# Optimization experiments

Hardware: AMD Instinct MI355X
Metric: run time of the kernel (lower is better)

## Reference

```python
import jax, jax.numpy as jnp
import numpy as np

B, S, D, C, H, E, K, L = 32, 512, 768, 3072, 1024, 8, 2, 2


def _layernorm(x, g, b, eps=1e-5):
    mu = jnp.mean(x, axis=-1, keepdims=True)
    var = jnp.var(x, axis=-1, keepdims=True)
    return (x - mu) * jax.lax.rsqrt(var + eps) * g + b


def setup_inputs() -> dict:
    key = jax.random.key(0)
    ks = jax.random.split(key, 12)
    s = 0.02
    return {
        "hidden_states": jax.random.normal(ks[0], (B, S, C), jnp.float32),
        "proj_w": jax.random.normal(ks[1], (C, D), jnp.float32) * s,
        "proj_b": jnp.zeros((D,), jnp.float32),
        "ln1_g": jnp.ones((D,), jnp.float32),
        "ln1_b": jnp.zeros((D,), jnp.float32),
        "gate_w": jax.random.normal(ks[2], (D, E), jnp.float32) * s,
        "gate_b": jnp.zeros((E,), jnp.float32),
        "w1": jax.random.normal(ks[3], (E, D, H), jnp.float32) * s,
        "b1": jnp.zeros((E, H), jnp.float32),
        "w2": jax.random.normal(ks[4], (E, H, D), jnp.float32) * s,
        "b2": jnp.zeros((E, D), jnp.float32),
        "ln2_g": jnp.ones((D,), jnp.float32),
        "ln2_b": jnp.zeros((D,), jnp.float32),
        "cls_w": jax.random.normal(ks[5], (D, L), jnp.float32) * s,
        "cls_b": jnp.zeros((L,), jnp.float32),
    }


def reference(hidden_states, proj_w, proj_b, ln1_g, ln1_b, gate_w, gate_b,
              w1, b1, w2, b2, ln2_g, ln2_b, cls_w, cls_b):
    # layer_projection: Linear -> LayerNorm -> GELU (dropout = identity in eval)
    x = jnp.einsum('bsc,cd->bsd', hidden_states, proj_w) + proj_b
    x = _layernorm(x, ln1_g, ln1_b)
    seq_out = jax.nn.gelu(x, approximate=False)  # [B,S,D]

    # Router: gate -> softmax -> top-k -> renormalize
    probs = jax.nn.softmax(seq_out @ gate_w + gate_b, axis=-1)  # [B,S,E]
    top_w, top_i = jax.lax.top_k(probs, K)                      # [B,S,K]
    top_w = top_w / jnp.sum(top_w, axis=-1, keepdims=True)

    # combine[t,e] = sum_k top_w[t,k] * (top_i[t,k]==e)
    combine = jnp.sum(jax.nn.one_hot(top_i, E, dtype=top_w.dtype)
                      * top_w[..., None], axis=-2)              # [B,S,E]

    xt = seq_out.reshape(-1, D)                                 # [T,D]
    ct = combine.reshape(-1, E)                                 # [T,E]
    h = jax.nn.gelu(jnp.einsum('td,edh->eth', xt, w1) + b1[:, None, :],
                    approximate=False)                          # [E,T,H]
    eo = jnp.einsum('eth,ehd->etd', h, w2) + b2[:, None, :]     # [E,T,D]
    moe = jnp.einsum('etd,te->td', eo, ct).reshape(B, S, D)

    moe = _layernorm(moe + seq_out, ln2_g, ln2_b)
    logits = moe @ cls_w + cls_b                                # [B,S,2]
    return logits
```

## Files before the change

### kernel.cpp

```cpp
#include <hip/hip_runtime.h>
#include <hip/hip_bf16.h>

#define T_TOK 16384
#define CDIM 3072
#define DDIM 768
#define HDIM 1024
#define NEXP 8
#define NSLOT 33792
#define MAXTILE 264
#define AMB_CAP 2048
#define AMB2_CAP 256
#define KSPLIT 4
#define NSEG 8

typedef __attribute__((ext_vector_type(8))) short bfrag;
typedef __attribute__((ext_vector_type(4))) float f32x4;
typedef __attribute__((ext_vector_type(4))) float fvec4;

__device__ __forceinline__ unsigned short bf16_rn(float f) {
  union { float f; unsigned u; } v; v.f = f;
  unsigned r = v.u + 0x7fffu + ((v.u >> 16) & 1u);
  return (unsigned short)(r >> 16);
}
__device__ __forceinline__ float bf16_f32(unsigned short h) {
  union { unsigned u; float f; } v; v.u = ((unsigned)h) << 16;
  return v.f;
}
__device__ __forceinline__ float gelu_exact(float x) {
  return 0.5f * x * (1.0f + erff(x * 0.70710678118654752440f));
}
__device__ __forceinline__ void glds16(const void* g, void* l) {
  __builtin_amdgcn_global_load_lds((const __attribute__((address_space(1))) void*)g,
                                   (__attribute__((address_space(3))) void*)l, 16, 0, 0);
}

__global__ void k_init(int* token_list, int* counts, int* cursors, unsigned short* zero_row,
                       int* amb_count, int* amb2_count) {
  int i = blockIdx.x * 256 + threadIdx.x;
  for (int j = i; j < NSLOT; j += 64 * 256) token_list[j] = -1;
  if (i < NEXP) counts[i] = 0;
  if (i < 128) cursors[i] = 0;
  if (i == 0) { *amb_count = 0; *amb2_count = 0; }
  if (i < 1024) zero_row[i] = 0;
}

__global__ void k_cast_tiled(const float* __restrict__ src,
                             unsigned short* __restrict__ dst) {
  __shared__ unsigned short h[128][136];
  int rb = blockIdx.x;
  int cc = blockIdx.y;
  int tid = threadIdx.x;
  const float* in = src + ((size_t)rb * 128) * CDIM + cc * 128;
#pragma unroll
  for (int it = 0; it < 16; ++it) {
    int idx = it * 256 + tid;
    int r = idx >> 5, nv = idx & 31;
    fvec4 v = *(const fvec4*)(in + (size_t)r * CDIM + nv * 4);
    unsigned long long p = (unsigned long long)bf16_rn(v[0]) |
                           ((unsigned long long)bf16_rn(v[1]) << 16) |
                           ((unsigned long long)bf16_rn(v[2]) << 32) |
                           ((unsigned long long)bf16_rn(v[3]) << 48);
    *(unsigned long long*)&h[r][nv * 4] = p;
  }
  __syncthreads();
  unsigned short* ob = dst + ((size_t)rb * 96 + cc * 4) * 4096;
#pragma unroll
  for (int kt = 0; kt < 4; ++kt) {
#pragma unroll
    for (int it = 0; it < 2; ++it) {
      int gg = it * 256 + tid;
      int kg = gg >> 7, r = gg & 127;
      bfrag o = *(const bfrag*)&h[r][kt * 32 + kg * 8];
      *(bfrag*)(ob + ((size_t)kt * 512 + gg) * 8) = o;
    }
  }
}

__global__ void k_transpose_split(const float* __restrict__ src,
                                  unsigned short* __restrict__ dhi,
                                  unsigned short* __restrict__ dlo) {
  __shared__ unsigned short h[128][72], l[128][72];
  int nb2 = blockIdx.x;
  int cb = blockIdx.y;
  int col_blk = nb2 >> 1, nhalf = nb2 & 1;
  int n0 = col_blk * 128 + nhalf * 64;
  int tid = threadIdx.x;
  const float* in = src + (size_t)(cb * 128) * DDIM + n0;
#pragma unroll
  for (int it = 0; it < 8; ++it) {
    int idx = it * 256 + tid;
    int cl = idx >> 4, nv = idx & 15;
    fvec4 v = *(const fvec4*)(in + (size_t)cl * DDIM + nv * 4);
    unsigned long long ph = 0, pl = 0;
#pragma unroll
    for (int e = 0; e < 4; ++e) {
      unsigned short hh = bf16_rn(v[e]);
      unsigned short ll = bf16_rn(v[e] - bf16_f32(hh));
      ph |= (unsigned long long)hh << (16 * e);
      pl |= (unsigned long long)ll << (16 * e);
    }
    *(unsigned long long*)&h[cl][nv * 4] = ph;
    *(unsigned long long*)&l[cl][nv * 4] = pl;
  }
  __syncthreads();
  size_t obase = ((size_t)col_blk * 96 + cb * 4) * 4096;
#pragma unroll
  for (int kt = 0; kt < 4; ++kt) {
    int kg = tid >> 6, rl = tid & 63;
    bfrag oh, ol;
#pragma unroll
    for (int e = 0; e < 8; ++e) {
      int c = kt * 32 + kg * 8 + e;
      oh[e] = (short)h[c][rl];
      ol[e] = (short)l[c][rl];
    }
    size_t gi = obase + ((size_t)kt * 512 + kg * 128 + nhalf * 64 + rl) * 8;
    *(bfrag*)(dhi + gi) = oh;
    *(bfrag*)(dlo + gi) = ol;
  }
}

__global__ void k_transpose_tiled(const float* __restrict__ src0,
                                  unsigned short* __restrict__ dst0, int K, int N) {
  __shared__ unsigned short h[128][72];
  int nb2 = blockIdx.x;
  int cb = blockIdx.y;
  int z = blockIdx.z;
  int col_blk = nb2 >> 1, nhalf = nb2 & 1;
  int n0 = col_blk * 128 + nhalf * 64;
  int tid = threadIdx.x;
  const float* in = src0 + (size_t)z * K * N + (size_t)(cb * 128) * N + n0;
#pragma unroll
  for (int it = 0; it < 8; ++it) {
    int idx = it * 256 + tid;
    int cl = idx >> 4, nv = idx & 15;
    fvec4 v = *(const fvec4*)(in + (size_t)cl * N + nv * 4);
    unsigned long long ph = 0;
#pragma unroll
    for (int e = 0; e < 4; ++e)
      ph |= (unsigned long long)bf16_rn(v[e]) << (16 * e);
    *(unsigned long long*)&h[cl][nv * 4] = ph;
  }
  __syncthreads();
  size_t obase = (size_t)z * K * N + ((size_t)col_blk * (K / 32) + cb * 4) * 4096;
#pragma unroll
  for (int kt = 0; kt < 4; ++kt) {
    int kg = tid >> 6, rl = tid & 63;
    bfrag oh;
#pragma unroll
    for (int e = 0; e < 8; ++e) oh[e] = (short)h[kt * 32 + kg * 8 + e][rl];
    *(bfrag*)(dst0 + obase + ((size_t)kt * 512 + kg * 128 + nhalf * 64 + rl) * 8) = oh;
  }
}

__launch_bounds__(256, 3)
__global__ void k_gemm1(const unsigned short* __restrict__ Atil,
                        const unsigned short* __restrict__ Btil,
                        float* __restrict__ Cout)
{
  __shared__ unsigned short sA[12288], sB[12288];
  int tid = threadIdx.x;
  int lane = tid & 63, wave = tid >> 6;
  int id = blockIdx.x;
  int swz = (id & 7) * 96 + (id >> 3);
  int brow = swz / 6, bcol = swz % 6;
  int row0 = brow * 128, col0 = bcol * 128;
  int wm = wave >> 1, wn = wave & 1;

  f32x4 acc[4][4];
#pragma unroll
  for (int i = 0; i < 4; ++i)
#pragma unroll
    for (int j = 0; j < 4; ++j) acc[i][j] = (f32x4){0.f, 0.f, 0.f, 0.f};

  int rsel = lane & 15, kq = lane >> 4;
  const unsigned short* At = Atil + (size_t)(brow * 96) * 4096;
  const unsigned short* Bt = Btil + (size_t)(bcol * 96) * 4096;

  auto STAGE = [&](int kt, int b) {
    const unsigned short* as = At + (size_t)kt * 4096;
    const unsigned short* bs = Bt + (size_t)kt * 4096;
    int lbase = b * 4096;
#pragma unroll
    for (int pass = 0; pass < 2; ++pass) {
      int g = pass * 256 + tid;
      int li = lbase + (pass * 256 + wave * 64) * 8;
      glds16(as + (size_t)g * 8, &sA[li]);
      glds16(bs + (size_t)g * 8, &sB[li]);
    }
  };

  STAGE(0, 0);
  STAGE(1, 1);
  int b0 = 0;
  for (int kt = 0; kt < 96; ++kt) {
    if (kt < 95) asm volatile("s_waitcnt vmcnt(4)" ::: "memory");
    else         asm volatile("s_waitcnt vmcnt(0)" ::: "memory");
    __builtin_amdgcn_s_barrier();
    if (kt + 2 < 96) {
      int bn = b0 + 2; if (bn >= 3) bn -= 3;
      STAGE(kt + 2, bn);
    }
    int lb = b0 * 4096;
    bfrag af[4], bf[4];
#pragma unroll
    for (int i = 0; i < 4; ++i) {
      af[i] = *(const bfrag*)&sA[lb + (kq * 128 + wm * 64 + i * 16 + rsel) * 8];
      bf[i] = *(const bfrag*)&sB[lb + (kq * 128 + wn * 64 + i * 16 + rsel) * 8];
    }
#pragma unroll
    for (int i = 0; i < 4; ++i)
#pragma unroll
      for (int j = 0; j < 4; ++j)
        acc[i][j] = __builtin_amdgcn_mfma_f32_16x16x32_bf16(af[i], bf[j], acc[i][j], 0, 0, 0);
    b0 = (b0 == 2) ? 0 : b0 + 1;
  }

  int cc = lane & 15, rr = (lane >> 4) * 4;
#pragma unroll
  for (int i = 0; i < 4; ++i)
#pragma unroll
    for (int j = 0; j < 4; ++j)
#pragma unroll
      for (int r = 0; r < 4; ++r) {
        int row = row0 + wm * 64 + i * 16 + rr + r;
        int col = col0 + wn * 64 + j * 16 + cc;
        Cout[(size_t)row * DDIM + col] = acc[i][j][r];
      }
}

__launch_bounds__(256)
__global__ void k_ln_router(const float* __restrict__ xw, const float* __restrict__ proj_b,
                            const float* __restrict__ g1, const float* __restrict__ b1v,
                            const float* __restrict__ gate_w, const float* __restrict__ gate_b,
                            unsigned short* __restrict__ seq_b16,
                            int* __restrict__ top_i, float* __restrict__ top_w,
                            int* __restrict__ amb_list, int* __restrict__ amb_count)
{
  int lane = threadIdx.x & 63;
  int t = blockIdx.x * 4 + (threadIdx.x >> 6);
  const float* xr = xw + (size_t)t * DDIM;
  float x0[12];
  float s = 0.f, s2 = 0.f;
#pragma unroll
  for (int j = 0; j < 12; ++j) {
    int d = lane + 64 * j;
    float v = xr[d] + proj_b[d];
    x0[j] = v; s += v; s2 += v * v;
  }
#pragma unroll
  for (int o = 32; o > 0; o >>= 1) { s += __shfl_xor(s, o, 64); s2 += __shfl_xor(s2, o, 64); }
  float mu = s * (1.f / DDIM);
  float rstd = rsqrtf(s2 * (1.f / DDIM) - mu * mu + 1e-5f);
  float acc8[8];
#pragma unroll
  for (int e = 0; e < 8; ++e) acc8[e] = 0.f;
#pragma unroll
  for (int j = 0; j < 12; ++j) {
    int d = lane + 64 * j;
    float y = (x0[j] - mu) * rstd * g1[d] + b1v[d];
    float ge = gelu_exact(y);
    seq_b16[(size_t)t * DDIM + d] = bf16_rn(ge);
    const float* gw = gate_w + (size_t)d * NEXP;
#pragma unroll
    for (int e = 0; e < 8; ++e) acc8[e] += ge * gw[e];
  }
#pragma unroll
  for (int e = 0; e < 8; ++e)
#pragma unroll
    for (int o = 32; o > 0; o >>= 1) acc8[e] += __shfl_xor(acc8[e], o, 64);
  if (lane == 0) {
    float lg[8];
#pragma unroll
    for (int e = 0; e < 8; ++e) lg[e] = acc8[e] + gate_b[e];
    int i0 = 0;
    for (int e = 1; e < 8; ++e) if (lg[e] > lg[i0]) i0 = e;
    int i1 = (i0 == 0) ? 1 : 0;
    for (int e = 0; e < 8; ++e) if (e != i0 && lg[e] > lg[i1]) i1 = e;
    float l2 = -1e30f;
    for (int e = 0; e < 8; ++e) if (e != i0 && e != i1 && lg[e] > l2) l2 = lg[e];
    if (lg[i1] - l2 < 8e-3f) {
      int p = atomicAdd(amb_count, 1);
      if (p < AMB_CAP) amb_list[p] = t;
    }
    float w0 = 1.f / (1.f + expf(lg[i1] - lg[i0]));
    top_i[t * 2] = i0; top_i[t * 2 + 1] = i1;
    top_w[t * 2] = w0; top_w[t * 2 + 1] = 1.f - w0;
  }
}

__launch_bounds__(256, 2)
__global__ void k_repair(const float* __restrict__ hidden,
                         const unsigned short* __restrict__ BTh,
                         const unsigned short* __restrict__ BTl,
                         const int* __restrict__ amb_list, const int* __restrict__ amb_count,
                         float* __restrict__ xw_fix4)
{
  int n = *amb_count; if (n > AMB_CAP) n = AMB_CAP;
  int by = blockIdx.y;
  if (by * 128 >= n) return;
  int bx = blockIdx.x;
  int z = blockIdx.z;
  int col0 = bx * 128;
  __shared__ unsigned short sAh[8192], sAl[8192], sBh[8192], sBl[8192];
  __shared__ int tk[128];
  int tid = threadIdx.x, lane = tid & 63, wave = tid >> 6;
  if (tid < 128) tk[tid] = (by * 128 + tid < n) ? amb_list[by * 128 + tid] : -1;
  __syncthreads();
  int wm = wave >> 1, wn = wave & 1;
  f32x4 acc[4][4];
#pragma unroll
  for (int i = 0; i < 4; ++i)
#pragma unroll
    for (int j = 0; j < 4; ++j) acc[i][j] = (f32x4){0.f, 0.f, 0.f, 0.f};
  int rsel = lane & 15, kq = lane >> 4;
  int ktbase = z * 24;
  const unsigned short* Bth = BTh + (size_t)(bx * 96) * 4096;
  const unsigned short* Btl = BTl + (size_t)(bx * 96) * 4096;

  auto STAGE = [&](int kt, int b) {
    int k0 = (ktbase + kt) * 32;
    int lb = b * 4096;
    size_t tb = (size_t)(ktbase + kt) * 4096;
#pragma unroll
    for (int pass = 0; pass < 2; ++pass) {
      int g = pass * 256 + tid;
      int kg = g >> 7, r = g & 127;
      int tok = tk[r];
      fvec4 a0 = (fvec4){0.f, 0.f, 0.f, 0.f}, a1 = a0;
      if (tok >= 0) {
        const float* ap = hidden + (size_t)tok * CDIM + k0 + kg * 8;
        a0 = *(const fvec4*)ap;
        a1 = *(const fvec4*)(ap + 4);
      }
      bfrag hv, lv;
#pragma unroll
      for (int u = 0; u < 8; ++u) {
        float v = (u < 4) ? a0[u] : a1[u - 4];
        unsigned short h = bf16_rn(v);
        hv[u] = (short)h;
        lv[u] = (short)bf16_rn(v - bf16_f32(h));
      }
      *(bfrag*)&sAh[lb + (size_t)g * 8] = hv;
      *(bfrag*)&sAl[lb + (size_t)g * 8] = lv;
      int li = lb + (pass * 256 + wave * 64) * 8;
      glds16(Bth + tb + (size_t)g * 8, &sBh[li]);
      glds16(Btl + tb + (size_t)g * 8, &sBl[li]);
    }
  };

  STAGE(0, 0);
  __syncthreads();
  for (int kt = 0; kt < 24; ++kt) {
    int b = kt & 1;
    if (kt + 1 < 24) STAGE(kt + 1, b ^ 1);
    int lb = b * 4096;
    bfrag ah[4], al[4], bh[4], bl[4];
#pragma unroll
    for (int i = 0; i < 4; ++i) {
      int ra = wm * 64 + i * 16 + rsel;
      ah[i] = *(const bfrag*)&sAh[lb + (kq * 128 + ra) * 8];
      al[i] = *(const bfrag*)&sAl[lb + (kq * 128 + ra) * 8];
      int cb = wn * 64 + i * 16 + rsel;
      bh[i] = *(const bfrag*)&sBh[lb + (kq * 128 + cb) * 8];
      bl[i] = *(const bfrag*)&sBl[lb + (kq * 128 + cb) * 8];
    }
#pragma unroll
    for (int i = 0; i < 4; ++i)
#pragma unroll
      for (int j = 0; j < 4; ++j) {
        acc[i][j] = __builtin_amdgcn_mfma_f32_16x16x32_bf16(ah[i], bh[j], acc[i][j], 0, 0, 0);
        acc[i][j] = __builtin_amdgcn_mfma_f32_16x16x32_bf16(ah[i], bl[j], acc[i][j], 0, 0, 0);
        acc[i][j] = __builtin_amdgcn_mfma_f32_16x16x32_bf16(al[i], bh[j], acc[i][j], 0, 0, 0);
      }
    __syncthreads();
  }
  float* dst = xw_fix4 + (size_t)z * AMB_CAP * DDIM;
  int cc = lane & 15, rr = (lane >> 4) * 4;
#pragma unroll
  for (int i = 0; i < 4; ++i)
#pragma unroll
    for (int j = 0; j < 4; ++j)
#pragma unroll
      for (int r = 0; r < 4; ++r) {
        int row = by * 128 + wm * 64 + i * 16 + rr + r;
        int col = col0 + wn * 64 + j * 16 + cc;
        dst[(size_t)row * DDIM + col] = acc[i][j][r];
      }
}

__launch_bounds__(256)
__global__ void k_fix2(const float* __restrict__ xw_fix4, const float* __restrict__ proj_b,
                       const float* __restrict__ g1, const float* __restrict__ b1v,
                       const float* __restrict__ gate_w, const float* __restrict__ gate_b,
                       const int* __restrict__ amb_list, const int* __restrict__ amb_count,
                       int* __restrict__ top_i, float* __restrict__ top_w,
                       int* __restrict__ amb2_list, int* __restrict__ amb2_count)
{
  int n = *amb_count; if (n > AMB_CAP) n = AMB_CAP;
  int lane = threadIdx.x & 63;
  int slot = blockIdx.x * 4 + (threadIdx.x >> 6);
  if (slot >= n) return;
  int t = amb_list[slot];
  const float* p0 = xw_fix4 + (size_t)slot * DDIM;
  const float* p1 = p0 + (size_t)AMB_CAP * DDIM;
  const float* p2 = p1 + (size_t)AMB_CAP * DDIM;
  const float* p3 = p2 + (size_t)AMB_CAP * DDIM;
  float x0[12];
  float s = 0.f, s2 = 0.f;
#pragma unroll
  for (int j = 0; j < 12; ++j) {
    int d = lane + 64 * j;
    float v = ((p0[d] + p1[d]) + (p2[d] + p3[d])) + proj_b[d];
    x0[j] = v; s += v; s2 += v * v;
  }
#pragma unroll
  for (int o = 32; o > 0; o >>= 1) { s += __shfl_xor(s, o, 64); s2 += __shfl_xor(s2, o, 64); }
  float mu = s * (1.f / DDIM);
  float rstd = rsqrtf(s2 * (1.f / DDIM) - mu * mu + 1e-5f);
  float acc8[8];
#pragma unroll
  for (int e = 0; e < 8; ++e) acc8[e] = 0.f;
#pragma unroll
  for (int j = 0; j < 12; ++j) {
    int d = lane + 64 * j;
    float y = (x0[j] - mu) * rstd * g1[d] + b1v[d];
    float ge = gelu_exact(y);
    const float* gw = gate_w + (size_t)d * NEXP;
#pragma unroll
    for (int e = 0; e < 8; ++e) acc8[e] += ge * gw[e];
  }
#pragma unroll
  for (int e = 0; e < 8; ++e)
#pragma unroll
    for (int o = 32; o > 0; o >>= 1) acc8[e] += __shfl_xor(acc8[e], o, 64);
  if (lane == 0) {
    float lg[8];
#pragma unroll
    for (int e = 0; e < 8; ++e) lg[e] = acc8[e] + gate_b[e];
    int i0 = 0;
    for (int e = 1; e < 8; ++e) if (lg[e] > lg[i0]) i0 = e;
    int i1 = (i0 == 0) ? 1 : 0;
    for (int e = 0; e < 8; ++e) if (e != i0 && lg[e] > lg[i1]) i1 = e;
    float l2 = -1e30f;
    for (int e = 0; e < 8; ++e) if (e != i0 && e != i1 && lg[e] > l2) l2 = lg[e];
    if (lg[i1] - l2 < 2e-4f) {
      int p = atomicAdd(amb2_count, 1);
      if (p < AMB2_CAP) amb2_list[p] = t;
    }
    float w0 = 1.f / (1.f + expf(lg[i1] - lg[i0]));
    top_i[t * 2] = i0; top_i[t * 2 + 1] = i1;
    top_w[t * 2] = w0; top_w[t * 2 + 1] = 1.f - w0;
  }
}

__launch_bounds__(256, 1)
__global__ void k_router_fix(const float* __restrict__ hidden, const float* __restrict__ proj_w,
                             const int* __restrict__ amb2_list, const int* __restrict__ amb2_count,
                             double* __restrict__ xpart)
{
  __shared__ float hrow[384];
  int tid = threadIdx.x;
  int seg = blockIdx.y;
  int cbase = seg * 384;
  int n = *amb2_count; if (n > AMB2_CAP) n = AMB2_CAP;
  for (int ii = blockIdx.x; ii < n; ii += gridDim.x) {
    int t = amb2_list[ii];
    __syncthreads();
    if (tid < 96)
      *(fvec4*)&hrow[tid * 4] = *(const fvec4*)(hidden + (size_t)t * CDIM + cbase + tid * 4);
    __syncthreads();
    double p0a = 0.0, p0b = 0.0, p1a = 0.0, p1b = 0.0, p2a = 0.0, p2b = 0.0;
    for (int c0 = 0; c0 < 384; c0 += 16) {
      float w0r[16], w1r[16], w2r[16];
      const float* wp = proj_w + (size_t)(cbase + c0) * DDIM + tid;
#pragma unroll
      for (int u = 0; u < 16; ++u) {
        w0r[u] = wp[u * DDIM];
        w1r[u] = wp[u * DDIM + 256];
        w2r[u] = wp[u * DDIM + 512];
      }
#pragma unroll
      for (int u = 0; u < 16; ++u) {
        double h = (double)hrow[c0 + u];
        if (u & 1) { p0b += h * (double)w0r[u]; p1b += h * (double)w1r[u]; p2b += h * (double)w2r[u]; }
        else       { p0a += h * (double)w0r[u]; p1a += h * (double)w1r[u]; p2a += h * (double)w2r[u]; }
      }
    }
    double* xp = xpart + ((size_t)seg * AMB2_CAP + ii) * DDIM;
    xp[tid] = p0a + p0b;
    xp[tid + 256] = p1a + p1b;
    xp[tid + 512] = p2a + p2b;
  }
}

__launch_bounds__(256)
__global__ void k_fix3(const double* __restrict__ xpart, const float* __restrict__ proj_b,
                       const float* __restrict__ g1, const float* __restrict__ b1v,
                       const float* __restrict__ gate_w, const float* __restrict__ gate_b,
                       const int* __restrict__ amb2_list, const int* __restrict__ amb2_count,
                       int* __restrict__ top_i, float* __restrict__ top_w)
{
  __shared__ double redA[4], redB[4], red8[4][8];
  int n = *amb2_count; if (n > AMB2_CAP) n = AMB2_CAP;
  int ii = blockIdx.x;
  if (ii >= n) return;
  int t = amb2_list[ii];
  int tid = threadIdx.x, lane = tid & 63, wave = tid >> 6;
  double x[3]; double s = 0.0, s2 = 0.0;
#pragma unroll
  for (int j = 0; j < 3; ++j) {
    int d = tid + 256 * j;
    double acc = (double)proj_b[d];
#pragma unroll
    for (int seg = 0; seg < NSEG; ++seg)
      acc += xpart[((size_t)seg * AMB2_CAP + ii) * DDIM + d];
    x[j] = acc; s += acc; s2 += acc * acc;
  }
#pragma unroll
  for (int o = 32; o > 0; o >>= 1) { s += __shfl_down(s, o, 64); s2 += __shfl_down(s2, o, 64); }
  if (lane == 0) { redA[wave] = s; redB[wave] = s2; }
  __syncthreads();
  double mu = (redA[0] + redA[1] + redA[2] + redA[3]) / DDIM;
  double ms = (redB[0] + redB[1] + redB[2] + redB[3]) / DDIM;
  double rstd = 1.0 / sqrt(ms - mu * mu + 1e-5);
  double a8[8];
#pragma unroll
  for (int e = 0; e < 8; ++e) a8[e] = 0.0;
#pragma unroll
  for (int j = 0; j < 3; ++j) {
    int d = tid + 256 * j;
    double y = (x[j] - mu) * rstd * (double)g1[d] + (double)b1v[d];
    double ge = 0.5 * y * (1.0 + erf(y * 0.7071067811865475244));
#pragma unroll
    for (int e = 0; e < 8; ++e) a8[e] += ge * (double)gate_w[(size_t)d * NEXP + e];
  }
#pragma unroll
  for (int e = 0; e < 8; ++e)
#pragma unroll
    for (int o = 32; o > 0; o >>= 1) a8[e] += __shfl_down(a8[e], o, 64);
  if (lane == 0) {
#pragma unroll
    for (int e = 0; e < 8; ++e) red8[wave][e] = a8[e];
  }
  __syncthreads();
  if (tid == 0) {
    double lg[8];
#pragma unroll
    for (int e = 0; e < 8; ++e)
      lg[e] = red8[0][e] + red8[1][e] + red8[2][e] + red8[3][e] + (double)gate_b[e];
    int i0 = 0;
    for (int e = 1; e < 8; ++e) if (lg[e] > lg[i0]) i0 = e;
    int i1 = (i0 == 0) ? 1 : 0;
    for (int e = 0; e < 8; ++e) if (e != i0 && e != i1 && lg[e] > lg[i1]) i1 = e;
    double w0 = 1.0 / (1.0 + exp(lg[i1] - lg[i0]));
    top_i[t * 2] = i0; top_i[t * 2 + 1] = i1;
    top_w[t * 2] = (float)w0; top_w[t * 2 + 1] = (float)(1.0 - w0);
  }
}

__global__ void k_count(const int* __restrict__ top_i, int* __restrict__ counts) {
  __shared__ int h[NEXP];
  int tid = threadIdx.x;
  if (tid < NEXP) h[tid] = 0;
  __syncthreads();
  for (int i = blockIdx.x * 256 + tid; i < 2 * T_TOK; i += 64 * 256)
    atomicAdd(&h[top_i[i]], 1);
  __syncthreads();
  if (tid < NEXP) atomicAdd(&counts[tid], h[tid]);
}

__global__ void k_offsets(const int* __restrict__ counts, int* __restrict__ seg_start,
                          int* __restrict__ padded_total, int* __restrict__ tile_expert) {
  if (threadIdx.x != 0 || blockIdx.x != 0) return;
  int st[NEXP], en[NEXP];
  int s = 0;
  for (int e = 0; e < NEXP; ++e) {
    st[e] = s; seg_start[e] = s;
    s += (counts[e] + 127) & ~127;
    en[e] = s;
  }
  *padded_total = s;
  int nt = s >> 7;
  for (int x = 0; x < nt; ++x) {
    int r = x << 7, e = 0;
    for (int q = 0; q < NEXP; ++q) if (r >= st[q] && r < en[q]) e = q;
    tile_expert[x] = e;
  }
}

__global__ void k_scatter(const int* __restrict__ top_i, const int* __restrict__ seg_start,
                          int* __restrict__ cursors, int* __restrict__ token_list,
                          int* __restrict__ slot_of) {
  __shared__ int lc[NEXP];
  __shared__ int lbase[NEXP];
  int tid = threadIdx.x;
  int t = blockIdx.x * 256 + tid;
  if (tid < NEXP) lc[tid] = 0;
  __syncthreads();
  int e0 = top_i[t * 2], e1 = top_i[t * 2 + 1];
  int o0 = atomicAdd(&lc[e0], 1);
  int o1 = atomicAdd(&lc[e1], 1);
  __syncthreads();
  if (tid < NEXP) lbase[tid] = atomicAdd(&cursors[tid << 4], lc[tid]);
  __syncthreads();
  int p0 = seg_start[e0] + lbase[e0] + o0;
  int p1 = seg_start[e1] + lbase[e1] + o1;
  token_list[p0] = t;
  token_list[p1] = t;
  slot_of[t * 2] = p0;
  slot_of[t * 2 + 1] = p1;
}

__global__ void k_gather(const unsigned short* __restrict__ seqb,
                         const int* __restrict__ token_list,
                         const int* __restrict__ padded_total,
                         unsigned short* __restrict__ seqgT) {
  int sb = blockIdx.x;
  if (sb * 128 >= *padded_total) return;
  int cc = blockIdx.y;
  __shared__ unsigned short h[128][136];
  __shared__ int tk[128];
  int tid = threadIdx.x;
  if (tid < 128) tk[tid] = token_list[sb * 128 + tid];
  __syncthreads();
#pragma unroll
  for (int it = 0; it < 8; ++it) {
    int idx = it * 256 + tid;
    int r = idx >> 4, nv = idx & 15;
    int tok = tk[r];
    bfrag v = (bfrag){0, 0, 0, 0, 0, 0, 0, 0};
    if (tok >= 0)
      v = *(const bfrag*)(seqb + (size_t)tok * DDIM + cc * 128 + nv * 8);
    *(bfrag*)&h[r][nv * 8] = v;
  }
  __syncthreads();
  unsigned short* ob = seqgT + ((size_t)sb * 24 + cc * 4) * 4096;
#pragma unroll
  for (int kt = 0; kt < 4; ++kt) {
#pragma unroll
    for (int it = 0; it < 2; ++it) {
      int gg = it * 256 + tid;
      int kg = gg >> 7, r = gg & 127;
      bfrag o = *(const bfrag*)&h[r][kt * 32 + kg * 8];
      *(bfrag*)(ob + ((size_t)kt * 512 + gg) * 8) = o;
    }
  }
}

__launch_bounds__(256, 4)
__global__ void k_gemm2(const unsigned short* __restrict__ seqgT,
                        const unsigned short* __restrict__ w1T,
                        const float* __restrict__ b1,
                        const int* __restrict__ tile_expert,
                        const int* __restrict__ padded_total,
                        unsigned short* __restrict__ hbufT)
{
  int by = blockIdx.x;
  if (by * 128 >= *padded_total) return;
  int bx = blockIdx.y;
  int e = tile_expert[by];
  __shared__ unsigned short sA[8192], sB[8192];
  int tid = threadIdx.x, lane = tid & 63, wave = tid >> 6;
  int col0 = bx * 128;
  int wm = wave >> 1, wn = wave & 1;
  f32x4 acc[4][4];
#pragma unroll
  for (int i = 0; i < 4; ++i)
#pragma unroll
    for (int j = 0; j < 4; ++j) acc[i][j] = (f32x4){0.f, 0.f, 0.f, 0.f};
  const unsigned short* At = seqgT + (size_t)by * 24 * 4096;
  const unsigned short* Bt = w1T + (size_t)e * HDIM * DDIM + (size_t)bx * 24 * 4096;
  int rsel = lane & 15, kq = lane >> 4;

  auto STAGE = [&](int kt, int b) {
    int lbase2 = b * 4096;
    size_t tb = (size_t)kt * 4096;
#pragma unroll
    for (int pass = 0; pass < 2; ++pass) {
      int g = pass * 256 + tid;
      int li = lbase2 + (pass * 256 + wave * 64) * 8;
      glds16(At + tb + (size_t)g * 8, &sA[li]);
      glds16(Bt + tb + (size_t)g * 8, &sB[li]);
    }
  };

  STAGE(0, 0);
  __syncthreads();
  for (int kt = 0; kt < 24; ++kt) {
    int b = kt & 1;
    if (kt + 1 < 24) STAGE(kt + 1, b ^ 1);
    int lb = b * 4096;
    bfrag af[4], bf[4];
#pragma unroll
    for (int i = 0; i < 4; ++i) {
      af[i] = *(const bfrag*)&sA[lb + (kq * 128 + wm * 64 + i * 16 + rsel) * 8];
      bf[i] = *(const bfrag*)&sB[lb + (kq * 128 + wn * 64 + i * 16 + rsel) * 8];
    }
#pragma unroll
    for (int i = 0; i < 4; ++i)
#pragma unroll
      for (int j = 0; j < 4; ++j)
        acc[i][j] = __builtin_amdgcn_mfma_f32_16x16x32_bf16(af[i], bf[j], acc[i][j], 0, 0, 0);
    __syncthreads();
  }
  int cc = lane & 15, rr = (lane >> 4) * 4;
#pragma unroll
  for (int i = 0; i < 4; ++i)
#pragma unroll
    for (int j = 0; j < 4; ++j)
#pragma unroll
      for (int r = 0; r < 4; ++r) {
        int lr = wm * 64 + i * 16 + rr + r;
        int col = col0 + wn * 64 + j * 16 + cc;
        float x = acc[i][j][r] + b1[(size_t)e * HDIM + col];
        size_t tile = (size_t)by * 32 + (col >> 5);
        int g = ((col >> 3) & 3) * 128 + lr;
        hbufT[tile * 4096 + g * 8 + (col & 7)] = bf16_rn(gelu_exact(x));
      }
}

__launch_bounds__(256, 4)
__global__ void k_gemm3(const unsigned short* __restrict__ hbufT,
                        const unsigned short* __restrict__ w2T,
                        const float* __restrict__ b2,
                        const int* __restrict__ tile_expert,
                        const int* __restrict__ padded_total,
                        float* __restrict__ eo)
{
  int by = blockIdx.x;
  if (by * 128 >= *padded_total) return;
  int bx = blockIdx.y;
  int e = tile_expert[by];
  __shared__ unsigned short sA[8192], sB[8192];
  int tid = threadIdx.x, lane = tid & 63, wave = tid >> 6;
  int col0 = bx * 128;
  int wm = wave >> 1, wn = wave & 1;
  f32x4 acc[4][4];
#pragma unroll
  for (int i = 0; i < 4; ++i)
#pragma unroll
    for (int j = 0; j < 4; ++j) acc[i][j] = (f32x4){0.f, 0.f, 0.f, 0.f};
  const unsigned short* At = hbufT + (size_t)by * 32 * 4096;
  const unsigned short* Bt = w2T + (size_t)e * DDIM * HDIM + (size_t)bx * 32 * 4096;
  int rsel = lane & 15, kq = lane >> 4;

  auto STAGE = [&](int kt, int b) {
    int lbase2 = b * 4096;
    size_t tb = (size_t)kt * 4096;
#pragma unroll
    for (int pass = 0; pass < 2; ++pass) {
      int g = pass * 256 + tid;
      int li = lbase2 + (pass * 256 + wave * 64) * 8;
      glds16(At + tb + (size_t)g * 8, &sA[li]);
      glds16(Bt + tb + (size_t)g * 8, &sB[li]);
    }
  };

  STAGE(0, 0);
  __syncthreads();
  for (int kt = 0; kt < 32; ++kt) {
    int b = kt & 1;
    if (kt + 1 < 32) STAGE(kt + 1, b ^ 1);
    int lb = b * 4096;
    bfrag af[4], bf[4];
#pragma unroll
    for (int i = 0; i < 4; ++i) {
      af[i] = *(const bfrag*)&sA[lb + (kq * 128 + wm * 64 + i * 16 + rsel) * 8];
      bf[i] = *(const bfrag*)&sB[lb + (kq * 128 + wn * 64 + i * 16 + rsel) * 8];
    }
#pragma unroll
    for (int i = 0; i < 4; ++i)
#pragma unroll
      for (int j = 0; j < 4; ++j)
        acc[i][j] = __builtin_amdgcn_mfma_f32_16x16x32_bf16(af[i], bf[j], acc[i][j], 0, 0, 0);
    __syncthreads();
  }
  int cc = lane & 15, rr = (lane >> 4) * 4;
#pragma unroll
  for (int i = 0; i < 4; ++i)
#pragma unroll
    for (int j = 0; j < 4; ++j)
#pragma unroll
      for (int r = 0; r < 4; ++r) {
        int row = by * 128 + wm * 64 + i * 16 + rr + r;
        int col = col0 + wn * 64 + j * 16 + cc;
        eo[(size_t)row * DDIM + col] = acc[i][j][r] + b2[(size_t)e * DDIM + col];
      }
}

__launch_bounds__(256)
__global__ void k_combine(const float* __restrict__ eo, const unsigned short* __restrict__ seqb,
                          const int* __restrict__ slot_of, const float* __restrict__ top_w,
                          const float* __restrict__ g2, const float* __restrict__ b2v,
                          const float* __restrict__ cls_w, const float* __restrict__ cls_b,
                          float* __restrict__ out)
{
  int lane = threadIdx.x & 63;
  int t = blockIdx.x * 4 + (threadIdx.x >> 6);
  int s0 = slot_of[t * 2], s1 = slot_of[t * 2 + 1];
  float w0 = top_w[t * 2], w1 = top_w[t * 2 + 1];
  const float* p0 = eo + (size_t)s0 * DDIM;
  const float* p1 = eo + (size_t)s1 * DDIM;
  const unsigned short* sq = seqb + (size_t)t * DDIM;
  float m[12];
  float s = 0.f, s2 = 0.f;
#pragma unroll
  for (int j = 0; j < 12; ++j) {
    int d = lane + 64 * j;
    float v = w0 * p0[d] + w1 * p1[d] + bf16_f32(sq[d]);
    m[j] = v; s += v; s2 += v * v;
  }
#pragma unroll
  for (int o = 32; o > 0; o >>= 1) { s += __shfl_xor(s, o, 64); s2 += __shfl_xor(s2, o, 64); }
  float mu = s * (1.f / DDIM);
  float rstd = rsqrtf(s2 * (1.f / DDIM) - mu * mu + 1e-5f);
  float l0 = 0.f, l1 = 0.f;
#pragma unroll
  for (int j = 0; j < 12; ++j) {
    int d = lane + 64 * j;
    float y = (m[j] - mu) * rstd * g2[d] + b2v[d];
    l0 += y * cls_w[d * 2];
    l1 += y * cls_w[d * 2 + 1];
  }
#pragma unroll
  for (int o = 32; o > 0; o >>= 1) { l0 += __shfl_xor(l0, o, 64); l1 += __shfl_xor(l1, o, 64); }
  if (lane == 0) {
    out[(size_t)t * 2] = l0 + cls_b[0];
    out[(size_t)t * 2 + 1] = l1 + cls_b[1];
  }
}

extern "C" void kernel_launch(void* const* d_in, const int* in_sizes, int n_in,
                              void* d_out, int out_size, void* d_ws, size_t ws_size,
                              hipStream_t stream) {
  const float* hidden = (const float*)d_in[0];
  const float* proj_w = (const float*)d_in[1];
  const float* proj_b = (const float*)d_in[2];
  const float* ln1_g  = (const float*)d_in[3];
  const float* ln1_b  = (const float*)d_in[4];
  const float* gate_w = (const float*)d_in[5];
  const float* gate_b = (const float*)d_in[6];
  const float* w1     = (const float*)d_in[7];
  const float* b1     = (const float*)d_in[8];
  const float* w2     = (const float*)d_in[9];
  const float* b2     = (const float*)d_in[10];
  const float* ln2_g  = (const float*)d_in[11];
  const float* ln2_b  = (const float*)d_in[12];
  const float* cls_w  = (const float*)d_in[13];
  const float* cls_b  = (const float*)d_in[14];
  float* out = (float*)d_out;

  char* base = (char*)d_ws;
  size_t off = 0;
  auto alloc = [&](size_t b) -> void* {
    void* p = base + off;
    off += (b + 255) & ~(size_t)255;
    return p;
  };
  unsigned short* pwT_hi = (unsigned short*)alloc((size_t)DDIM * CDIM * 2);
  unsigned short* pwT_lo = (unsigned short*)alloc((size_t)DDIM * CDIM * 2);
  unsigned short* w1T    = (unsigned short*)alloc((size_t)NEXP * HDIM * DDIM * 2);
  unsigned short* w2T    = (unsigned short*)alloc((size_t)NEXP * DDIM * HDIM * 2);
  float* xw              = (float*)alloc((size_t)T_TOK * DDIM * 4);
  float* xw_fix4         = (float*)alloc((size_t)KSPLIT * AMB_CAP * DDIM * 4);
  double* xpart          = (double*)alloc((size_t)NSEG * AMB2_CAP * DDIM * 8);
  unsigned short* seqb   = (unsigned short*)alloc((size_t)T_TOK * DDIM * 2);
  unsigned short* seqgT  = (unsigned short*)alloc((size_t)MAXTILE * 24 * 4096 * 2);
  int* top_i             = (int*)alloc((size_t)T_TOK * 2 * 4);
  float* top_w           = (float*)alloc((size_t)T_TOK * 2 * 4);
  int* slot_of           = (int*)alloc((size_t)T_TOK * 2 * 4);
  int* amb_list          = (int*)alloc((size_t)AMB_CAP * 4);
  int* amb2_list         = (int*)alloc((size_t)AMB2_CAP * 4);
  int* token_list        = (int*)alloc((size_t)NSLOT * 4);
  int* counts            = (int*)alloc(256);
  int* cursors           = (int*)alloc(512);
  int* seg_start         = (int*)alloc(256);
  int* padded_total      = (int*)alloc(256);
  int* tile_expert       = (int*)alloc((size_t)MAXTILE * 4);
  unsigned short* zero_row = (unsigned short*)alloc(2048);
  int* amb_count         = (int*)alloc(256);
  int* amb2_count        = (int*)alloc(256);
  size_t poolBytes = 2 * (size_t)T_TOK * CDIM * 2;
  char* pool = (char*)alloc(poolBytes);
  unsigned short* Ahi = (unsigned short*)pool;
  size_t poff = 0;
  auto palloc = [&](size_t b) -> void* {
    void* p = pool + poff;
    poff += (b + 255) & ~(size_t)255;
    return p;
  };
  unsigned short* hbufT  = (unsigned short*)palloc((size_t)MAXTILE * 32 * 4096 * 2);
  float* eo              = (float*)palloc((size_t)NSLOT * DDIM * 4);
  (void)ws_size; (void)in_sizes; (void)n_in; (void)out_size;

  k_init<<<64, 256, 0, stream>>>(token_list, counts, cursors, zero_row, amb_count, amb2_count);
  k_cast_tiled<<<dim3(128, 24), 256, 0, stream>>>(hidden, Ahi);
  k_transpose_split<<<dim3(12, 24), 256, 0, stream>>>(proj_w, pwT_hi, pwT_lo);
  k_transpose_tiled<<<dim3(16, 6, 8), 256, 0, stream>>>(w1, w1T, DDIM, HDIM);
  k_transpose_tiled<<<dim3(12, 8, 8), 256, 0, stream>>>(w2, w2T, HDIM, DDIM);
  k_gemm1<<<768, 256, 0, stream>>>(Ahi, pwT_hi, xw);
  k_ln_router<<<T_TOK / 4, 256, 0, stream>>>(xw, proj_b, ln1_g, ln1_b, gate_w, gate_b,
                                             seqb, top_i, top_w, amb_list, amb_count);
  k_repair<<<dim3(6, AMB_CAP / 128, KSPLIT), 256, 0, stream>>>(hidden, pwT_hi, pwT_lo,
                                                               amb_list, amb_count, xw_fix4);
  k_fix2<<<AMB_CAP / 4, 256, 0, stream>>>(xw_fix4, proj_b, ln1_g, ln1_b, gate_w, gate_b,
                                          amb_list, amb_count, top_i, top_w,
                                          amb2_list, amb2_count);
  k_router_fix<<<dim3(64, NSEG), 256, 0, stream>>>(hidden, proj_w, amb2_list, amb2_count, xpart);
  k_fix3<<<AMB2_CAP, 256, 0, stream>>>(xpart, proj_b, ln1_g, ln1_b, gate_w, gate_b,
                                       amb2_list, amb2_count, top_i, top_w);
  k_count<<<64, 256, 0, stream>>>(top_i, counts);
  k_offsets<<<1, 64, 0, stream>>>(counts, seg_start, padded_total, tile_expert);
  k_scatter<<<64, 256, 0, stream>>>(top_i, seg_start, cursors, token_list, slot_of);
  k_gather<<<dim3(MAXTILE, 6), 256, 0, stream>>>(seqb, token_list, padded_total, seqgT);
  k_gemm2<<<dim3(MAXTILE, 8), 256, 0, stream>>>(seqgT, w1T, b1, tile_expert,
                                                padded_total, hbufT);
  k_gemm3<<<dim3(MAXTILE, 6), 256, 0, stream>>>(hbufT, w2T, b2, tile_expert, padded_total, eo);
  k_combine<<<T_TOK / 4, 256, 0, stream>>>(eo, seqb, slot_of, top_w, ln2_g, ln2_b,
                                           cls_w, cls_b, out);
}
```

Baseline: 631.7 us.

## Widen expert GEMM tiles to 128x256 and store expert outputs in bf16

Both expert GEMMs now compute 128x256 output tiles per block, with each wave covering 64x128, so A-tile loads are reused across twice as many columns and the grid's column dimension is halved. Launch bounds drop to 2 blocks per CU to make room for the larger accumulator array and doubled B shared memory. Separately, the expert output buffer is stored as bf16 instead of fp32, halving the write traffic in gemm3 and the read traffic in the combine kernel. The cost is fewer resident waves, fewer blocks to fill the GPU, and some loss of precision in the expert outputs.

```diff
diff --git a/kernel.cpp b/kernel.cpp
--- a/kernel.cpp
+++ b/kernel.cpp
@@ -648,7 +648,7 @@
   }
 }
 
-__launch_bounds__(256, 4)
+__launch_bounds__(256, 2)
 __global__ void k_gemm2(const unsigned short* __restrict__ seqgT,
                         const unsigned short* __restrict__ w1T,
                         const float* __restrict__ b1,
@@ -660,28 +660,32 @@
   if (by * 128 >= *padded_total) return;
   int bx = blockIdx.y;
   int e = tile_expert[by];
-  __shared__ unsigned short sA[8192], sB[8192];
+  __shared__ unsigned short sA[8192], sB[16384];
   int tid = threadIdx.x, lane = tid & 63, wave = tid >> 6;
-  int col0 = bx * 128;
   int wm = wave >> 1, wn = wave & 1;
-  f32x4 acc[4][4];
+  f32x4 acc[4][8];
 #pragma unroll
   for (int i = 0; i < 4; ++i)
 #pragma unroll
-    for (int j = 0; j < 4; ++j) acc[i][j] = (f32x4){0.f, 0.f, 0.f, 0.f};
+    for (int j = 0; j < 8; ++j) acc[i][j] = (f32x4){0.f, 0.f, 0.f, 0.f};
   const unsigned short* At = seqgT + (size_t)by * 24 * 4096;
-  const unsigned short* Bt = w1T + (size_t)e * HDIM * DDIM + (size_t)bx * 24 * 4096;
+  const unsigned short* Bt0 = w1T + (size_t)e * HDIM * DDIM + (size_t)(2 * bx) * 24 * 4096;
+  const unsigned short* Bt1 = Bt0 + (size_t)24 * 4096;
   int rsel = lane & 15, kq = lane >> 4;
 
   auto STAGE = [&](int kt, int b) {
-    int lbase2 = b * 4096;
     size_t tb = (size_t)kt * 4096;
 #pragma unroll
-    for (int pass = 0; pass < 2; ++pass) {
-      int g = pass * 256 + tid;
-      int li = lbase2 + (pass * 256 + wave * 64) * 8;
-      glds16(At + tb + (size_t)g * 8, &sA[li]);
-      glds16(Bt + tb + (size_t)g * 8, &sB[li]);
+    for (int p = 0; p < 2; ++p) {
+      int li = b * 4096 + (p * 256 + wave * 64) * 8;
+      glds16(At + tb + (size_t)(p * 256 + tid) * 8, &sA[li]);
+    }
+#pragma unroll
+    for (int p = 0; p < 4; ++p) {
+      const unsigned short* src = (p < 2) ? Bt0 : Bt1;
+      int gg = (p & 1) * 256 + tid;
+      int li = b * 8192 + ((p >= 2) ? 4096 : 0) + ((p & 1) * 256 + wave * 64) * 8;
+      glds16(src + tb + (size_t)gg * 8, &sB[li]);
     }
   };
 
@@ -690,17 +694,19 @@
   for (int kt = 0; kt < 24; ++kt) {
     int b = kt & 1;
     if (kt + 1 < 24) STAGE(kt + 1, b ^ 1);
-    int lb = b * 4096;
-    bfrag af[4], bf[4];
-#pragma unroll
-    for (int i = 0; i < 4; ++i) {
-      af[i] = *(const bfrag*)&sA[lb + (kq * 128 + wm * 64 + i * 16 + rsel) * 8];
-      bf[i] = *(const bfrag*)&sB[lb + (kq * 128 + wn * 64 + i * 16 + rsel) * 8];
-    }
+    int lbA = b * 4096;
+    int lbB = b * 8192 + wn * 4096;
+    bfrag af[4], bf[8];
 #pragma unroll
     for (int i = 0; i < 4; ++i)
-#pragma unroll
-      for (int j = 0; j < 4; ++j)
+      af[i] = *(const bfrag*)&sA[lbA + (kq * 128 + wm * 64 + i * 16 + rsel) * 8];
+#pragma unroll
+    for (int j = 0; j < 8; ++j)
+      bf[j] = *(const bfrag*)&sB[lbB + (kq * 128 + j * 16 + rsel) * 8];
+#pragma unroll
+    for (int i = 0; i < 4; ++i)
+#pragma unroll
+      for (int j = 0; j < 8; ++j)
         acc[i][j] = __builtin_amdgcn_mfma_f32_16x16x32_bf16(af[i], bf[j], acc[i][j], 0, 0, 0);
     __syncthreads();
   }
@@ -708,52 +714,56 @@
 #pragma unroll
   for (int i = 0; i < 4; ++i)
 #pragma unroll
-    for (int j = 0; j < 4; ++j)
+    for (int j = 0; j < 8; ++j)
 #pragma unroll
       for (int r = 0; r < 4; ++r) {
         int lr = wm * 64 + i * 16 + rr + r;
-        int col = col0 + wn * 64 + j * 16 + cc;
-        float x = acc[i][j][r] + b1[(size_t)e * HDIM + col];
-        size_t tile = (size_t)by * 32 + (col >> 5);
-        int g = ((col >> 3) & 3) * 128 + lr;
-        hbufT[tile * 4096 + g * 8 + (col & 7)] = bf16_rn(gelu_exact(x));
+        int gcol = bx * 256 + wn * 128 + j * 16 + cc;
+        float x = acc[i][j][r] + b1[(size_t)e * HDIM + gcol];
+        size_t tile = (size_t)by * 32 + (gcol >> 5);
+        int g = ((gcol >> 3) & 3) * 128 + lr;
+        hbufT[tile * 4096 + g * 8 + (gcol & 7)] = bf16_rn(gelu_exact(x));
       }
 }
 
-__launch_bounds__(256, 4)
+__launch_bounds__(256, 2)
 __global__ void k_gemm3(const unsigned short* __restrict__ hbufT,
                         const unsigned short* __restrict__ w2T,
                         const float* __restrict__ b2,
                         const int* __restrict__ tile_expert,
                         const int* __restrict__ padded_total,
-                        float* __restrict__ eo)
+                        unsigned short* __restrict__ eo)
 {
   int by = blockIdx.x;
   if (by * 128 >= *padded_total) return;
   int bx = blockIdx.y;
   int e = tile_expert[by];
-  __shared__ unsigned short sA[8192], sB[8192];
+  __shared__ unsigned short sA[8192], sB[16384];
   int tid = threadIdx.x, lane = tid & 63, wave = tid >> 6;
-  int col0 = bx * 128;
   int wm = wave >> 1, wn = wave & 1;
-  f32x4 acc[4][4];
+  f32x4 acc[4][8];
 #pragma unroll
   for (int i = 0; i < 4; ++i)
 #pragma unroll
-    for (int j = 0; j < 4; ++j) acc[i][j] = (f32x4){0.f, 0.f, 0.f, 0.f};
+    for (int j = 0; j < 8; ++j) acc[i][j] = (f32x4){0.f, 0.f, 0.f, 0.f};
   const unsigned short* At = hbufT + (size_t)by * 32 * 4096;
-  const unsigned short* Bt = w2T + (size_t)e * DDIM * HDIM + (size_t)bx * 32 * 4096;
+  const unsigned short* Bt0 = w2T + (size_t)e * DDIM * HDIM + (size_t)(2 * bx) * 32 * 4096;
+  const unsigned short* Bt1 = Bt0 + (size_t)32 * 4096;
   int rsel = lane & 15, kq = lane >> 4;
 
   auto STAGE = [&](int kt, int b) {
-    int lbase2 = b * 4096;
     size_t tb = (size_t)kt * 4096;
 #pragma unroll
-    for (int pass = 0; pass < 2; ++pass) {
-      int g = pass * 256 + tid;
-      int li = lbase2 + (pass * 256 + wave * 64) * 8;
-      glds16(At + tb + (size_t)g * 8, &sA[li]);
-      glds16(Bt + tb + (size_t)g * 8, &sB[li]);
+    for (int p = 0; p < 2; ++p) {
+      int li = b * 4096 + (p * 256 + wave * 64) * 8;
+      glds16(At + tb + (size_t)(p * 256 + tid) * 8, &sA[li]);
+    }
+#pragma unroll
+    for (int p = 0; p < 4; ++p) {
+      const unsigned short* src = (p < 2) ? Bt0 : Bt1;
+      int gg = (p & 1) * 256 + tid;
+      int li = b * 8192 + ((p >= 2) ? 4096 : 0) + ((p & 1) * 256 + wave * 64) * 8;
+      glds16(src + tb + (size_t)gg * 8, &sB[li]);
     }
   };
 
@@ -762,17 +772,19 @@
   for (int kt = 0; kt < 32; ++kt) {
     int b = kt & 1;
     if (kt + 1 < 32) STAGE(kt + 1, b ^ 1);
-    int lb = b * 4096;
-    bfrag af[4], bf[4];
-#pragma unroll
-    for (int i = 0; i < 4; ++i) {
-      af[i] = *(const bfrag*)&sA[lb + (kq * 128 + wm * 64 + i * 16 + rsel) * 8];
-      bf[i] = *(const bfrag*)&sB[lb + (kq * 128 + wn * 64 + i * 16 + rsel) * 8];
-    }
+    int lbA = b * 4096;
+    int lbB = b * 8192 + wn * 4096;
+    bfrag af[4], bf[8];
 #pragma unroll
     for (int i = 0; i < 4; ++i)
-#pragma unroll
-      for (int j = 0; j < 4; ++j)
+      af[i] = *(const bfrag*)&sA[lbA + (kq * 128 + wm * 64 + i * 16 + rsel) * 8];
+#pragma unroll
+    for (int j = 0; j < 8; ++j)
+      bf[j] = *(const bfrag*)&sB[lbB + (kq * 128 + j * 16 + rsel) * 8];
+#pragma unroll
+    for (int i = 0; i < 4; ++i)
+#pragma unroll
+      for (int j = 0; j < 8; ++j)
         acc[i][j] = __builtin_amdgcn_mfma_f32_16x16x32_bf16(af[i], bf[j], acc[i][j], 0, 0, 0);
     __syncthreads();
   }
@@ -780,17 +792,19 @@
 #pragma unroll
   for (int i = 0; i < 4; ++i)
 #pragma unroll
-    for (int j = 0; j < 4; ++j)
+    for (int j = 0; j < 8; ++j)
 #pragma unroll
       for (int r = 0; r < 4; ++r) {
         int row = by * 128 + wm * 64 + i * 16 + rr + r;
-        int col = col0 + wn * 64 + j * 16 + cc;
-        eo[(size_t)row * DDIM + col] = acc[i][j][r] + b2[(size_t)e * DDIM + col];
+        int gcol = bx * 256 + wn * 128 + j * 16 + cc;
+        eo[(size_t)row * DDIM + gcol] =
+            bf16_rn(acc[i][j][r] + b2[(size_t)e * DDIM + gcol]);
       }
 }
 
 __launch_bounds__(256)
-__global__ void k_combine(const float* __restrict__ eo, const unsigned short* __restrict__ seqb,
+__global__ void k_combine(const unsigned short* __restrict__ eo,
+                          const unsigned short* __restrict__ seqb,
                           const int* __restrict__ slot_of, const float* __restrict__ top_w,
                           const float* __restrict__ g2, const float* __restrict__ b2v,
                           const float* __restrict__ cls_w, const float* __restrict__ cls_b,
@@ -800,15 +814,15 @@
   int t = blockIdx.x * 4 + (threadIdx.x >> 6);
   int s0 = slot_of[t * 2], s1 = slot_of[t * 2 + 1];
   float w0 = top_w[t * 2], w1 = top_w[t * 2 + 1];
-  const float* p0 = eo + (size_t)s0 * DDIM;
-  const float* p1 = eo + (size_t)s1 * DDIM;
+  const unsigned short* p0 = eo + (size_t)s0 * DDIM;
+  const unsigned short* p1 = eo + (size_t)s1 * DDIM;
   const unsigned short* sq = seqb + (size_t)t * DDIM;
   float m[12];
   float s = 0.f, s2 = 0.f;
 #pragma unroll
   for (int j = 0; j < 12; ++j) {
     int d = lane + 64 * j;
-    float v = w0 * p0[d] + w1 * p1[d] + bf16_f32(sq[d]);
+    float v = w0 * bf16_f32(p0[d]) + w1 * bf16_f32(p1[d]) + bf16_f32(sq[d]);
     m[j] = v; s += v; s2 += v * v;
   }
 #pragma unroll
@@ -891,7 +905,7 @@
     return p;
   };
   unsigned short* hbufT  = (unsigned short*)palloc((size_t)MAXTILE * 32 * 4096 * 2);
-  float* eo              = (float*)palloc((size_t)NSLOT * DDIM * 4);
+  unsigned short* eo     = (unsigned short*)palloc((size_t)NSLOT * DDIM * 2);
   (void)ws_size; (void)in_sizes; (void)n_in; (void)out_size;
 
   k_init<<<64, 256, 0, stream>>>(token_list, counts, cursors, zero_row, amb_count, amb2_count);
@@ -914,9 +928,9 @@
   k_offsets<<<1, 64, 0, stream>>>(counts, seg_start, padded_total, tile_expert);
   k_scatter<<<64, 256, 0, stream>>>(top_i, seg_start, cursors, token_list, slot_of);
   k_gather<<<dim3(MAXTILE, 6), 256, 0, stream>>>(seqb, token_list, padded_total, seqgT);
-  k_gemm2<<<dim3(MAXTILE, 8), 256, 0, stream>>>(seqgT, w1T, b1, tile_expert,
+  k_gemm2<<<dim3(MAXTILE, 4), 256, 0, stream>>>(seqgT, w1T, b1, tile_expert,
                                                 padded_total, hbufT);
-  k_gemm3<<<dim3(MAXTILE, 6), 256, 0, stream>>>(hbufT, w2T, b2, tile_expert, padded_total, eo);
+  k_gemm3<<<dim3(MAXTILE, 3), 256, 0, stream>>>(hbufT, w2T, b2, tile_expert, padded_total, eo);
   k_combine<<<T_TOK / 4, 256, 0, stream>>>(eo, seqb, slot_of, top_w, ln2_g, ln2_b,
                                            cls_w, cls_b, out);
 }
```

Result: slower. 732.9 us (+16.0%).
